# Kernel optimization log

Hardware: AMD Instinct MI355X
Metric: run time of the kernel (lower is better)

Reference implementation:

```python
import jax, jax.numpy as jnp
import numpy as np
from jax import lax

B, T, P, H, O = 64, 96, 256, 128, 24  # batch, seq_len, num_points, hidden_dim, pred_len


def setup_inputs() -> dict:
    key = jax.random.key(0)
    ks = jax.random.split(key, 7)
    s = 1.0 / np.sqrt(H)  # torch LSTM/Linear default init scale
    return {
        "x": jax.random.normal(ks[0], (B, T, P, 1), dtype=jnp.float32),
        "W_ih": jax.random.uniform(ks[1], (P, 4 * H, 1), jnp.float32, -s, s),
        "W_hh": jax.random.uniform(ks[2], (P, 4 * H, H), jnp.float32, -s, s),
        "b_ih": jax.random.uniform(ks[3], (P, 4 * H), jnp.float32, -s, s),
        "b_hh": jax.random.uniform(ks[4], (P, 4 * H), jnp.float32, -s, s),
        "W_fc": jax.random.uniform(ks[5], (P, O, H), jnp.float32, -s, s),
        "b_fc": jax.random.uniform(ks[6], (P, O), jnp.float32, -s, s),
    }


def reference(x, W_ih, W_hh, b_ih, b_hh, W_fc, b_fc):
    # x: [B, T, P, F]; model uses only feature 0
    xs = x[..., 0]  # [B, T, P]
    # input_dim == 1, so input-to-gate contribution is a scaled broadcast of W_ih
    # precompute for all timesteps: [T, B, P, 4H]
    gx = jnp.einsum("btp,pg->tbpg", xs, W_ih[:, :, 0]) + (b_ih + b_hh)

    def step(carry, gxt):
        h, c = carry  # [B, P, H] each
        gates = gxt + jnp.einsum("bph,pgh->bpg", h, W_hh)  # [B, P, 4H]
        i, f, g, o = jnp.split(gates, 4, axis=-1)  # torch gate order i,f,g,o
        i = jax.nn.sigmoid(i)
        f = jax.nn.sigmoid(f)
        g = jnp.tanh(g)
        o = jax.nn.sigmoid(o)
        c = f * c + i * g
        h = o * jnp.tanh(c)
        return (h, c), None

    h0 = jnp.zeros((B, P, H), dtype=x.dtype)
    (h, _), _ = lax.scan(step, (h0, h0), gx)
    # per-point Linear on final hidden state: [B, P, O]
    out = jnp.einsum("bph,poh->bpo", h, W_fc) + b_fc
    # original stacks point outputs on last dim -> [B, pred_len, P]
    return jnp.transpose(out, (0, 2, 1))
```

## Files before the change

kernel.cpp:

```cpp
#include <hip/hip_runtime.h>
#include <hip/hip_bf16.h>

#define Bdim 64
#define Tdim 96
#define Pdim 256
#define Hdim 128
#define Gdim 512
#define Odim 24
#define BH   32
#define WROW 132

typedef _Float16 f16x8 __attribute__((ext_vector_type(8)));
typedef float    f32x16 __attribute__((ext_vector_type(16)));
typedef float    f32x2  __attribute__((ext_vector_type(2)));

union H8 { uint2 u2[2]; unsigned short s[8]; _Float16 h[8]; f16x8 v; };
union HS { _Float16 h; unsigned short s; };

__device__ __forceinline__ float exp2_fast(float x) {
#if __has_builtin(__builtin_amdgcn_exp2f)
    return __builtin_amdgcn_exp2f(x);
#else
    return __expf(x * 0.6931471805599453f);
#endif
}

__global__ __launch_bounds__(1024, 4)
void lstm_fused(const float* __restrict__ x,
                const float* __restrict__ W_ih,
                const float* __restrict__ W_hh,
                const float* __restrict__ b_ih,
                const float* __restrict__ b_hh,
                const float* __restrict__ W_fc,
                const float* __restrict__ b_fc,
                float* __restrict__ out)
{
    __shared__ unsigned short hs[2][2][BH * WROW];

    const int p   = blockIdx.x;
    const int tid = threadIdx.x;
    const int w   = tid >> 6;
    const int l31 = tid & 31;
    const int hi  = (tid >> 5) & 1;

    const float L1 = 1.4426950408889634f;
    const float L2 = 2.0f * L1;

    for (int i = tid; i < 2 * 2 * BH * WROW; i += 1024) ((unsigned short*)hs)[i] = 0;

    f16x8 afr[9];
    {
        const int rp   = w * 32 + l31;
        const int orow = ((rp & 3) << 7) | (rp >> 2);
        const float sc = ((rp & 3) == 2) ? L2 : L1;
        const float* rowp = W_hh + (size_t)p * Gdim * Hdim + (size_t)orow * Hdim;
        #pragma unroll
        for (int ks = 0; ks < 8; ++ks) {
            int k0 = ks * 16 + hi * 8;
            float4 va = *(const float4*)(rowp + k0);
            float4 vb = *(const float4*)(rowp + k0 + 4);
            H8 u;
            u.h[0] = (_Float16)(sc * va.x); u.h[1] = (_Float16)(sc * va.y);
            u.h[2] = (_Float16)(sc * va.z); u.h[3] = (_Float16)(sc * va.w);
            u.h[4] = (_Float16)(sc * vb.x); u.h[5] = (_Float16)(sc * vb.y);
            u.h[6] = (_Float16)(sc * vb.z); u.h[7] = (_Float16)(sc * vb.w);
            afr[ks] = u.v;
        }
        H8 u9;
        #pragma unroll
        for (int j = 0; j < 8; ++j) u9.s[j] = 0;
        if (hi == 0) {
            u9.h[0] = (_Float16)(sc * W_ih[(size_t)p * Gdim + orow]);
            u9.h[1] = (_Float16)(sc * (b_ih[(size_t)p * Gdim + orow] +
                                       b_hh[(size_t)p * Gdim + orow]));
        }
        afr[8] = u9.v;
    }

    f32x16 zacc;
    #pragma unroll
    for (int j = 0; j < 16; ++j) zacc[j] = 0.f;

    f32x2 cre[4];
    #pragma unroll
    for (int q = 0; q < 4; ++q) cre[q] = f32x2{0.f, 0.f};

    const float* xp0 = x + (size_t)((0 * BH + l31) * Tdim) * Pdim + p;
    const float* xp1 = x + (size_t)((1 * BH + l31) * Tdim) * Pdim + p;
    float xv0 = xp0[0];
    float xv1 = xp1[0];

    const int lbase = l31 * (WROW * 2);

    __syncthreads();

    auto dostep = [&](const int cur, const int t) {
        float xn0 = 0.f, xn1 = 0.f;
        if (t + 1 < Tdim) {
            xn0 = xp0[(size_t)(t + 1) * Pdim];
            xn1 = xp1[(size_t)(t + 1) * Pdim];
        }

        const char* h0 = (const char*)hs[0][cur];
        const char* h1 = (const char*)hs[1][cur];
        f32x16 a0, a1;
        #pragma unroll
        for (int ks = 0; ks < 8; ++ks) {
            int boff = lbase + ks * 32 + hi * 16;
            H8 b0, b1;
            b0.u2[0] = *(const uint2*)(h0 + boff);
            b0.u2[1] = *(const uint2*)(h0 + boff + 8);
            b1.u2[0] = *(const uint2*)(h1 + boff);
            b1.u2[1] = *(const uint2*)(h1 + boff + 8);
            a0 = __builtin_amdgcn_mfma_f32_32x32x16_f16(afr[ks], b0.v, ks ? a0 : zacc, 0, 0, 0);
            a1 = __builtin_amdgcn_mfma_f32_32x32x16_f16(afr[ks], b1.v, ks ? a1 : zacc, 0, 0, 0);
        }
        {
            H8 bg0, bg1;
            #pragma unroll
            for (int j = 0; j < 8; ++j) { bg0.s[j] = 0; bg1.s[j] = 0; }
            if (hi == 0) {
                bg0.h[0] = (_Float16)xv0; bg0.h[1] = (_Float16)1.0f;
                bg1.h[0] = (_Float16)xv1; bg1.h[1] = (_Float16)1.0f;
            }
            a0 = __builtin_amdgcn_mfma_f32_32x32x16_f16(afr[8], bg0.v, a0, 0, 0, 0);
            a1 = __builtin_amdgcn_mfma_f32_32x32x16_f16(afr[8], bg1.v, a1, 0, 0, 0);
        }

        unsigned short* w0 = hs[0][cur ^ 1];
        unsigned short* w1 = hs[1][cur ^ 1];
        #pragma unroll
        for (int q = 0; q < 4; ++q) {
            f32x2 yi = {a0[4 * q + 0], a1[4 * q + 0]};
            f32x2 yf = {a0[4 * q + 1], a1[4 * q + 1]};
            f32x2 yg = {a0[4 * q + 2], a1[4 * q + 2]};
            f32x2 yo = {a0[4 * q + 3], a1[4 * q + 3]};
            f32x2 Ef = {exp2_fast(-yf.x), exp2_fast(-yf.y)};
            f32x2 Ei = {exp2_fast(-yi.x), exp2_fast(-yi.y)};
            f32x2 Eg = {exp2_fast(yg.x),  exp2_fast(yg.y)};
            f32x2 t1 = Ef + 1.0f;
            f32x2 t2 = Ei + 1.0f;
            f32x2 t3 = Eg + 1.0f;
            f32x2 t4 = Eg - 1.0f;
            f32x2 den = (t1 * t2) * t3;
            f32x2 num = (cre[q] * t2) * t3 + (L2 * t4) * t1;
            float D = den.x * den.y;
            float r = __builtin_amdgcn_rcpf(D);
            f32x2 inv = {r * den.y, r * den.x};
            f32x2 cn  = num * inv;
            cn.x = fminf(30.0f, fmaxf(-30.0f, cn.x));
            cn.y = fminf(30.0f, fmaxf(-30.0f, cn.y));
            cre[q] = cn;
            f32x2 Eo = {exp2_fast(-yo.x), exp2_fast(-yo.y)};
            f32x2 Ec = {exp2_fast(cn.x),  exp2_fast(cn.y)};
            f32x2 d2 = (Eo + 1.0f) * (Ec + 1.0f);
            float D2 = d2.x * d2.y;
            float r2 = __builtin_amdgcn_rcpf(D2);
            f32x2 j2 = {r2 * d2.y, r2 * d2.x};
            f32x2 hv = (Ec - 1.0f) * j2;
            HS ha; ha.h = (_Float16)hv.x;
            HS hb; hb.h = (_Float16)hv.y;
            int idx = l31 * WROW + (w * 8 + 2 * q + hi);
            w0[idx] = ha.s;
            w1[idx] = hb.s;
        }

        __syncthreads();
        xv0 = xn0; xv1 = xn1;
    };

    for (int t = 0; t < Tdim; t += 2) {
        dostep(0, t);
        dostep(1, t + 1);
    }

    const float* wfc = W_fc + (size_t)p * Odim * Hdim;
    const float* bfc = b_fc + (size_t)p * Odim;
    for (int i = tid; i < Bdim * Odim; i += 1024) {
        int o = i % Odim;
        int b = i / Odim;
        const unsigned short* hr = (b < BH) ? (hs[0][0] + b * WROW)
                                            : (hs[1][0] + (b - BH) * WROW);
        float s = bfc[o];
        const float* wr = wfc + o * Hdim;
        #pragma unroll 8
        for (int k2 = 0; k2 < Hdim; ++k2) {
            HS s2; s2.s = hr[k2];
            s = __builtin_fmaf(wr[k2], (float)s2.h, s);
        }
        out[(size_t)b * Odim * Pdim + (size_t)o * Pdim + p] = s;
    }
}

extern "C" void kernel_launch(void* const* d_in, const int* in_sizes, int n_in,
                              void* d_out, int out_size, void* d_ws, size_t ws_size,
                              hipStream_t stream) {
    const float* x    = (const float*)d_in[0];
    const float* W_ih = (const float*)d_in[1];
    const float* W_hh = (const float*)d_in[2];
    const float* b_ih = (const float*)d_in[3];
    const float* b_hh = (const float*)d_in[4];
    const float* W_fc = (const float*)d_in[5];
    const float* b_fc = (const float*)d_in[6];
    float* out = (float*)d_out;

    lstm_fused<<<dim3(Pdim), dim3(1024), 0, stream>>>(x, W_ih, W_hh, b_ih, b_hh, W_fc, b_fc, out);
}
```

Baseline: 408.5 us.

## Software-pipeline the two batch halves so one half's MFMA overlaps the other's gate math

Each LSTM step is split into two phases that alternate between the two 32-row batch halves. While the MFMA chain for one half's recurrent GEMM runs, the sigmoid/tanh epilogue for the other half executes, and sched_group_barrier hints interleave the MFMA, LDS and VALU instructions. Barriers per step double, but the matrix and vector units are meant to stay busy at the same time instead of running serially. The scheduling hints and reordered accumulator element mapping add fragility, and a redundant zero-init loop was added.

```diff
diff --git a/kernel.cpp b/kernel.cpp
--- a/kernel.cpp
+++ b/kernel.cpp
@@ -24,6 +24,8 @@
     return __expf(x * 0.6931471805599453f);
 #endif
 }
+
+#define SGB __builtin_amdgcn_sched_group_barrier
 
 __global__ __launch_bounds__(1024, 4)
 void lstm_fused(const float* __restrict__ x,
@@ -35,7 +37,8 @@
                 const float* __restrict__ b_fc,
                 float* __restrict__ out)
 {
-    __shared__ unsigned short hs[2][2][BH * WROW];
+    __shared__ unsigned short hb0[2][BH * WROW];
+    __shared__ unsigned short hb1[2][BH * WROW];
 
     const int p   = blockIdx.x;
     const int tid = threadIdx.x;
@@ -46,7 +49,15 @@
     const float L1 = 1.4426950408889634f;
     const float L2 = 2.0f * L1;
 
-    for (int i = tid; i < 2 * 2 * BH * WROW; i += 1024) ((unsigned short*)hs)[i] = 0;
+    for (int i = tid; i < 2 * BH * WROW; i += 1024) {
+        hb0[0][i < BH * WROW ? i : i - BH * WROW] = 0;
+    }
+    for (int i = tid; i < 2 * BH * WROW; i += 1024) {
+        ((unsigned short*)hb0)[i] = 0;
+    }
+    for (int i = tid; i < 2 * BH * WROW; i += 1024) {
+        ((unsigned short*)hb1)[i] = 0;
+    }
 
     f16x8 afr[9];
     {
@@ -77,101 +88,137 @@
         afr[8] = u9.v;
     }
 
-    f32x16 zacc;
+    const int lbase = l31 * (WROW * 2);
+
+    auto ldh = [&](const char* hb, int ks) -> H8 {
+        H8 r;
+        int boff = lbase + ks * 32 + hi * 16;
+        r.u2[0] = *(const uint2*)(hb + boff);
+        r.u2[1] = *(const uint2*)(hb + boff + 8);
+        return r;
+    };
+
+    auto ep_pair = [&](const f32x16& a, int j, f32x2* cr, unsigned short* wb) {
+        f32x2 yi = {a[8 * j + 0], a[8 * j + 4]};
+        f32x2 yf = {a[8 * j + 1], a[8 * j + 5]};
+        f32x2 yg = {a[8 * j + 2], a[8 * j + 6]};
+        f32x2 yo = {a[8 * j + 3], a[8 * j + 7]};
+        f32x2 Ef = {exp2_fast(-yf.x), exp2_fast(-yf.y)};
+        f32x2 Ei = {exp2_fast(-yi.x), exp2_fast(-yi.y)};
+        f32x2 Eg = {exp2_fast(yg.x),  exp2_fast(yg.y)};
+        f32x2 t1 = Ef + 1.0f;
+        f32x2 t2 = Ei + 1.0f;
+        f32x2 t3 = Eg + 1.0f;
+        f32x2 t4 = Eg - 1.0f;
+        f32x2 den = (t1 * t2) * t3;
+        f32x2 num = (cr[j] * t2) * t3 + (L2 * t4) * t1;
+        float D = den.x * den.y;
+        float r = __builtin_amdgcn_rcpf(D);
+        f32x2 inv = {r * den.y, r * den.x};
+        f32x2 cn  = num * inv;
+        cn.x = fminf(30.0f, fmaxf(-30.0f, cn.x));
+        cn.y = fminf(30.0f, fmaxf(-30.0f, cn.y));
+        cr[j] = cn;
+        f32x2 Eo = {exp2_fast(-yo.x), exp2_fast(-yo.y)};
+        f32x2 Ec = {exp2_fast(cn.x),  exp2_fast(cn.y)};
+        f32x2 d2 = (Eo + 1.0f) * (Ec + 1.0f);
+        float D2 = d2.x * d2.y;
+        float r2 = __builtin_amdgcn_rcpf(D2);
+        f32x2 j2 = {r2 * d2.y, r2 * d2.x};
+        f32x2 hv = (Ec - 1.0f) * j2;
+        HS ha; ha.h = (_Float16)hv.x;
+        HS hc; hc.h = (_Float16)hv.y;
+        int base = l31 * WROW + (w * 8 + 4 * j + hi);
+        wb[base]     = ha.s;
+        wb[base + 2] = hc.s;
+    };
+
+    auto phase = [&](const unsigned short* rb, unsigned short* wb,
+                     f32x16& aw, const f32x16& ar, f32x2* cr, float xv,
+                     bool doGemm, bool doEp) {
+        if (doGemm) {
+            const char* hb = (const char*)rb;
+            H8 f0 = ldh(hb, 0), f1 = ldh(hb, 1);
+            H8 f2 = ldh(hb, 2), f3 = ldh(hb, 3);
+            f32x16 z;
+            #pragma unroll
+            for (int j = 0; j < 16; ++j) z[j] = 0.f;
+            f32x16 a;
+            a = __builtin_amdgcn_mfma_f32_32x32x16_f16(afr[0], f0.v, z, 0, 0, 0);
+            a = __builtin_amdgcn_mfma_f32_32x32x16_f16(afr[1], f1.v, a, 0, 0, 0);
+            if (doEp) ep_pair(ar, 0, cr, wb);
+            H8 f4 = ldh(hb, 4), f5 = ldh(hb, 5);
+            a = __builtin_amdgcn_mfma_f32_32x32x16_f16(afr[2], f2.v, a, 0, 0, 0);
+            a = __builtin_amdgcn_mfma_f32_32x32x16_f16(afr[3], f3.v, a, 0, 0, 0);
+            if (doEp) ep_pair(ar, 1, cr, wb);
+            H8 f6 = ldh(hb, 6), f7 = ldh(hb, 7);
+            a = __builtin_amdgcn_mfma_f32_32x32x16_f16(afr[4], f4.v, a, 0, 0, 0);
+            a = __builtin_amdgcn_mfma_f32_32x32x16_f16(afr[5], f5.v, a, 0, 0, 0);
+            a = __builtin_amdgcn_mfma_f32_32x32x16_f16(afr[6], f6.v, a, 0, 0, 0);
+            a = __builtin_amdgcn_mfma_f32_32x32x16_f16(afr[7], f7.v, a, 0, 0, 0);
+            H8 bg;
+            #pragma unroll
+            for (int j = 0; j < 8; ++j) bg.s[j] = 0;
+            if (hi == 0) { bg.h[0] = (_Float16)xv; bg.h[1] = (_Float16)1.0f; }
+            a = __builtin_amdgcn_mfma_f32_32x32x16_f16(afr[8], bg.v, a, 0, 0, 0);
+            aw = a;
+            if (doEp) {
+                SGB(0x100, 2, 0);
+                SGB(0x008, 1, 0);
+                SGB(0x402, 25, 0);
+                SGB(0x100, 2, 0);
+                SGB(0x008, 1, 0);
+                SGB(0x402, 25, 0);
+                SGB(0x200, 2, 0);
+                SGB(0x100, 2, 0);
+                SGB(0x008, 2, 0);
+                SGB(0x402, 25, 0);
+                SGB(0x100, 2, 0);
+                SGB(0x008, 2, 0);
+                SGB(0x402, 25, 0);
+                SGB(0x200, 2, 0);
+                SGB(0x008, 3, 0);
+            }
+        } else if (doEp) {
+            ep_pair(ar, 0, cr, wb);
+            ep_pair(ar, 1, cr, wb);
+        }
+    };
+
+    f32x2 cre0[2] = {f32x2{0.f, 0.f}, f32x2{0.f, 0.f}};
+    f32x2 cre1[2] = {f32x2{0.f, 0.f}, f32x2{0.f, 0.f}};
+    f32x16 acc0, acc1;
     #pragma unroll
-    for (int j = 0; j < 16; ++j) zacc[j] = 0.f;
-
-    f32x2 cre[4];
-    #pragma unroll
-    for (int q = 0; q < 4; ++q) cre[q] = f32x2{0.f, 0.f};
+    for (int j = 0; j < 16; ++j) { acc0[j] = 0.f; acc1[j] = 0.f; }
 
     const float* xp0 = x + (size_t)((0 * BH + l31) * Tdim) * Pdim + p;
     const float* xp1 = x + (size_t)((1 * BH + l31) * Tdim) * Pdim + p;
-    float xv0 = xp0[0];
     float xv1 = xp1[0];
 
-    const int lbase = l31 * (WROW * 2);
-
     __syncthreads();
 
-    auto dostep = [&](const int cur, const int t) {
-        float xn0 = 0.f, xn1 = 0.f;
+    {
+        float xv0 = xp0[0];
+        phase(hb0[0], hb1[0], acc0, acc1, cre1, xv0, true, false);
+    }
+    __syncthreads();
+
+    for (int t = 0; t < Tdim; ++t) {
+        const int P  = t & 1;
+        const int tn = (t + 1 < Tdim) ? (t + 1) : t;
+        float xn0 = xp0[(size_t)tn * Pdim];
+
+        phase(hb1[P], hb0[P ^ 1], acc1, acc0, cre0, xv1, true, true);
+        __syncthreads();
+
+        float xn1 = xp1[(size_t)tn * Pdim];
         if (t + 1 < Tdim) {
-            xn0 = xp0[(size_t)(t + 1) * Pdim];
-            xn1 = xp1[(size_t)(t + 1) * Pdim];
-        }
-
-        const char* h0 = (const char*)hs[0][cur];
-        const char* h1 = (const char*)hs[1][cur];
-        f32x16 a0, a1;
-        #pragma unroll
-        for (int ks = 0; ks < 8; ++ks) {
-            int boff = lbase + ks * 32 + hi * 16;
-            H8 b0, b1;
-            b0.u2[0] = *(const uint2*)(h0 + boff);
-            b0.u2[1] = *(const uint2*)(h0 + boff + 8);
-            b1.u2[0] = *(const uint2*)(h1 + boff);
-            b1.u2[1] = *(const uint2*)(h1 + boff + 8);
-            a0 = __builtin_amdgcn_mfma_f32_32x32x16_f16(afr[ks], b0.v, ks ? a0 : zacc, 0, 0, 0);
-            a1 = __builtin_amdgcn_mfma_f32_32x32x16_f16(afr[ks], b1.v, ks ? a1 : zacc, 0, 0, 0);
-        }
-        {
-            H8 bg0, bg1;
-            #pragma unroll
-            for (int j = 0; j < 8; ++j) { bg0.s[j] = 0; bg1.s[j] = 0; }
-            if (hi == 0) {
-                bg0.h[0] = (_Float16)xv0; bg0.h[1] = (_Float16)1.0f;
-                bg1.h[0] = (_Float16)xv1; bg1.h[1] = (_Float16)1.0f;
-            }
-            a0 = __builtin_amdgcn_mfma_f32_32x32x16_f16(afr[8], bg0.v, a0, 0, 0, 0);
-            a1 = __builtin_amdgcn_mfma_f32_32x32x16_f16(afr[8], bg1.v, a1, 0, 0, 0);
-        }
-
-        unsigned short* w0 = hs[0][cur ^ 1];
-        unsigned short* w1 = hs[1][cur ^ 1];
-        #pragma unroll
-        for (int q = 0; q < 4; ++q) {
-            f32x2 yi = {a0[4 * q + 0], a1[4 * q + 0]};
-            f32x2 yf = {a0[4 * q + 1], a1[4 * q + 1]};
-            f32x2 yg = {a0[4 * q + 2], a1[4 * q + 2]};
-            f32x2 yo = {a0[4 * q + 3], a1[4 * q + 3]};
-            f32x2 Ef = {exp2_fast(-yf.x), exp2_fast(-yf.y)};
-            f32x2 Ei = {exp2_fast(-yi.x), exp2_fast(-yi.y)};
-            f32x2 Eg = {exp2_fast(yg.x),  exp2_fast(yg.y)};
-            f32x2 t1 = Ef + 1.0f;
-            f32x2 t2 = Ei + 1.0f;
-            f32x2 t3 = Eg + 1.0f;
-            f32x2 t4 = Eg - 1.0f;
-            f32x2 den = (t1 * t2) * t3;
-            f32x2 num = (cre[q] * t2) * t3 + (L2 * t4) * t1;
-            float D = den.x * den.y;
-            float r = __builtin_amdgcn_rcpf(D);
-            f32x2 inv = {r * den.y, r * den.x};
-            f32x2 cn  = num * inv;
-            cn.x = fminf(30.0f, fmaxf(-30.0f, cn.x));
-            cn.y = fminf(30.0f, fmaxf(-30.0f, cn.y));
-            cre[q] = cn;
-            f32x2 Eo = {exp2_fast(-yo.x), exp2_fast(-yo.y)};
-            f32x2 Ec = {exp2_fast(cn.x),  exp2_fast(cn.y)};
-            f32x2 d2 = (Eo + 1.0f) * (Ec + 1.0f);
-            float D2 = d2.x * d2.y;
-            float r2 = __builtin_amdgcn_rcpf(D2);
-            f32x2 j2 = {r2 * d2.y, r2 * d2.x};
-            f32x2 hv = (Ec - 1.0f) * j2;
-            HS ha; ha.h = (_Float16)hv.x;
-            HS hb; hb.h = (_Float16)hv.y;
-            int idx = l31 * WROW + (w * 8 + 2 * q + hi);
-            w0[idx] = ha.s;
-            w1[idx] = hb.s;
-        }
-
+            phase(hb0[P ^ 1], hb1[P ^ 1], acc0, acc1, cre1, xn0, true, true);
+        } else {
+            phase(hb0[P ^ 1], hb1[P ^ 1], acc0, acc1, cre1, 0.f, false, true);
+        }
         __syncthreads();
-        xv0 = xn0; xv1 = xn1;
-    };
-
-    for (int t = 0; t < Tdim; t += 2) {
-        dostep(0, t);
-        dostep(1, t + 1);
+        xv1 = xn1;
     }
 
     const float* wfc = W_fc + (size_t)p * Odim * Hdim;
@@ -179,8 +226,8 @@
     for (int i = tid; i < Bdim * Odim; i += 1024) {
         int o = i % Odim;
         int b = i / Odim;
-        const unsigned short* hr = (b < BH) ? (hs[0][0] + b * WROW)
-                                            : (hs[1][0] + (b - BH) * WROW);
+        const unsigned short* hr = (b < BH) ? (hb0[0] + b * WROW)
+                                            : (hb1[0] + (b - BH) * WROW);
         float s = bfc[o];
         const float* wr = wfc + o * Hdim;
         #pragma unroll 8
```

Result: faster. 399.2 us (-2.3%).
